# Optimization experiments

Measured on AMD Instinct MI355X. Metric: run time of the kernel, lower is better.

The kernel has to match this reference:

```python
import jax, jax.numpy as jnp
import numpy as np

EPS = 1e-5
KS = 3  # deformable kernel size
K2 = KS * KS


def conv2d(x, w, stride=1, padding=1):
    return jax.lax.conv_general_dilated(
        x, w, window_strides=(stride, stride),
        padding=[(padding, padding), (padding, padding)],
        dimension_numbers=("NCHW", "OIHW", "NCHW"))


def batchnorm(x, gamma, beta):
    # training-mode BN: batch statistics over (N, H, W)
    mean = jnp.mean(x, axis=(0, 2, 3), keepdims=True)
    var = jnp.var(x, axis=(0, 2, 3), keepdims=True)
    xhat = (x - mean) * jax.lax.rsqrt(var + EPS)
    return xhat * gamma[None, :, None, None] + beta[None, :, None, None]


def deform_conv(x, offsets, w, pad=1):
    # x: (B,C,H,W); offsets: (B,2*K2,H,W) -> first K2 channels = row (y)
    # offsets, next K2 = col (x) offsets; w: (O,C,KS,KS)
    B, C, H, W = x.shape
    xp = jnp.pad(x, ((0, 0), (0, 0), (pad, pad), (pad, pad)))
    Hp, Wp = H + 2 * pad, W + 2 * pad
    # base grid (center of each output pixel in padded coords)
    p0_y = jnp.arange(H, dtype=x.dtype) + pad            # (H,)
    p0_x = jnp.arange(W, dtype=x.dtype) + pad            # (W,)
    # kernel tap offsets in [-1, 0, 1]^2, row-major
    pn = jnp.stack(jnp.meshgrid(jnp.arange(KS) - pad, jnp.arange(KS) - pad,
                                indexing="ij"), axis=-1).reshape(K2, 2).astype(x.dtype)
    off = offsets.reshape(B, 2, K2, H, W)
    off_y = jnp.transpose(off[:, 0], (0, 2, 3, 1))       # (B,H,W,K2)
    off_x = jnp.transpose(off[:, 1], (0, 2, 3, 1))
    py = p0_y[None, :, None, None] + pn[:, 0][None, None, None, :] + off_y
    px = p0_x[None, None, :, None] + pn[:, 1][None, None, None, :] + off_x
    py = jnp.clip(py, 0.0, Hp - 1.0)
    px = jnp.clip(px, 0.0, Wp - 1.0)
    y0 = jnp.floor(py).astype(jnp.int32)
    x0 = jnp.floor(px).astype(jnp.int32)
    y1 = jnp.minimum(y0 + 1, Hp - 1)
    x1 = jnp.minimum(x0 + 1, Wp - 1)
    wy = (py - y0.astype(x.dtype))[:, None]              # (B,1,H,W,K2)
    wx = (px - x0.astype(x.dtype))[:, None]

    def gather(xb, yi, xi):                              # xb (C,Hp,Wp)
        return xb[:, yi, xi]                             # (C,H,W,K2)
    g = jax.vmap(gather)
    v00 = g(xp, y0, x0)
    v01 = g(xp, y0, x1)
    v10 = g(xp, y1, x0)
    v11 = g(xp, y1, x1)
    sampled = (v00 * (1 - wy) * (1 - wx) + v01 * (1 - wy) * wx +
               v10 * wy * (1 - wx) + v11 * wy * wx)      # (B,C,H,W,K2)
    return jnp.einsum("bchwk,ock->bohw", sampled, w.reshape(w.shape[0], C, K2))


def setup_inputs() -> dict:
    key = jax.random.key(0)
    ks = jax.random.split(key, 16)
    B, Cin, P, H, W = 64, 64, 64, 64, 64
    s = lambda k, shp, fan: jax.random.normal(k, shp, jnp.float32) * (fan ** -0.5)
    return {
        "x": jax.random.normal(ks[0], (B, Cin, H, W), jnp.float32),
        "conv1_w": s(ks[1], (P, Cin, 3, 3), Cin * 9),
        "bn1_g": jnp.ones((P,), jnp.float32), "bn1_b": jnp.zeros((P,), jnp.float32),
        "conv2_w": s(ks[2], (16, P, 1, 1), P),
        "bn2_g": jnp.ones((16,), jnp.float32), "bn2_b": jnp.zeros((16,), jnp.float32),
        "off_w": s(ks[3], (18, 16, 3, 3), 16 * 9) * 0.1,
        "off_b": jnp.zeros((18,), jnp.float32),
        "conv3_w": s(ks[4], (16, 16, 3, 3), 16 * 9),
        "bn3_g": jnp.ones((16,), jnp.float32), "bn3_b": jnp.zeros((16,), jnp.float32),
        "conv4_w": s(ks[5], (P, 16, 3, 3), 16 * 9),
        "bn4_g": jnp.ones((P,), jnp.float32), "bn4_b": jnp.zeros((P,), jnp.float32),
    }


def reference(x, conv1_w, bn1_g, bn1_b, conv2_w, bn2_g, bn2_b, off_w, off_b,
              conv3_w, bn3_g, bn3_b, conv4_w, bn4_g, bn4_b):
    out = jax.nn.relu(batchnorm(conv2d(x, conv1_w, 1, 1), bn1_g, bn1_b))
    out = jax.nn.relu(batchnorm(conv2d(out, conv2_w, 1, 0), bn2_g, bn2_b))
    offsets = conv2d(out, off_w, 1, 1) + off_b[None, :, None, None]
    out = jax.nn.relu(batchnorm(deform_conv(out, offsets, conv3_w), bn3_g, bn3_b))
    out = batchnorm(conv2d(out, conv4_w, 1, 1), bn4_g, bn4_b)
    out = out + x  # identity shortcut (stride=1, in_planes==planes)
    return jax.nn.relu(out)
```

## Files before the change

kernel.cpp:

```cpp
#include <hip/hip_runtime.h>

#define BN_N 262144.0f

typedef unsigned short u16;
typedef __attribute__((ext_vector_type(8))) short short8;
typedef __attribute__((ext_vector_type(4))) float floatx4;

#define RP1 4224
#define IS1 278784
#define RP2 1584
#define IS2 104544
#define H2P_TOTAL 6690816

static __device__ __forceinline__ u16 f2bf(float f) {
  union { float f; unsigned u; } v; v.f = f;
  unsigned u = v.u;
  return (u16)((u + 0x7FFFu + ((u >> 16) & 1u)) >> 16);
}
static __device__ __forceinline__ float bf2f(u16 h) {
  union { unsigned u; float f; } v; v.u = ((unsigned)h) << 16;
  return v.f;
}
static __device__ __forceinline__ void cp16(const u16* g, u16* l) {
  __builtin_amdgcn_global_load_lds((const __attribute__((address_space(1))) unsigned int*)g,
                                   (__attribute__((address_space(3))) unsigned int*)l, 16, 0, 0);
}

__global__ __launch_bounds__(256) void prep_w_k(const float* __restrict__ w1,
                                                u16* __restrict__ Bsw) {
  int d = blockIdx.x * 256 + threadIdx.x;
  int kin = d & 7, n = (d >> 3) & 63, kgrp = (d >> 9) & 3, kc = d >> 11;
  int k = kc * 32 + kgrp * 8 + kin;
  int tap = k >> 6, c = k & 63;
  Bsw[d] = f2bf(w1[n * 576 + c * 9 + tap]);
}

__global__ __launch_bounds__(256) void prep_w4_k(const float* __restrict__ w4,
                                                 u16* __restrict__ Bsw4) {
  int d = blockIdx.x * 256 + threadIdx.x;
  if (d >= 10240) return;
  int kin = d & 7, n = (d >> 3) & 63, lk = (d >> 9) & 3, kk = d >> 11;
  int tap = kk * 2 + (lk >> 1);
  int c = ((lk & 1) << 3) + kin;
  float v = (tap < 9) ? w4[n * 144 + c * 9 + tap] : 0.f;
  Bsw4[d] = f2bf(v);
}

__global__ __launch_bounds__(256) void prep_w3_k(const float* __restrict__ w3,
                                                 u16* __restrict__ Bsw3) {
  int d = blockIdx.x * 256 + threadIdx.x;
  if (d >= 2560) return;
  int kin = d & 7, n = (d >> 3) & 15, lk = (d >> 7) & 3, kk = d >> 9;
  int k = kk * 32 + lk * 8 + kin;
  int tap = k >> 4, c = k & 15;
  float v = (tap < 9) ? w3[n * 144 + c * 9 + tap] : 0.f;
  Bsw3[d] = f2bf(v);
}

__global__ __launch_bounds__(256) void prep_wo_k(const float* __restrict__ ow,
                                                 u16* __restrict__ BswO) {
  int d = blockIdx.x * 256 + threadIdx.x;
  if (d >= 5120) return;
  int kin = d & 7, n = (d >> 3) & 31, lk = (d >> 8) & 3, kk = d >> 10;
  int tap = kk * 2 + (lk >> 1);
  int c = ((lk & 1) << 3) + kin;
  float v = (tap < 9 && n < 18) ? ow[n * 144 + c * 9 + tap] : 0.f;
  BswO[d] = f2bf(v);
}

__global__ __launch_bounds__(256) void prep_x_k(const float* __restrict__ x,
                                                u16* __restrict__ xp) {
  int yp = blockIdx.x;
  int b = blockIdx.y;
  int tid = threadIdx.x;
  u16* rowbase = xp + (size_t)(b * 66 + yp) * RP1;
  if (yp == 0 || yp == 65) {
    for (int i = tid; i < RP1 / 4; i += 256)
      ((ushort4*)rowbase)[i] = make_ushort4(0, 0, 0, 0);
    return;
  }
  int y = yp - 1;
  __shared__ __align__(16) u16 s[64][72];
  for (int i = tid; i < 4096; i += 256) {
    int c = i >> 6, xx = i & 63;
    s[xx][c] = f2bf(x[((b * 64 + c) << 12) + (y << 6) + xx]);
  }
  if (tid < 128) {
    int c = tid & 63;
    int pxp = (tid >> 6) ? 65 : 0;
    rowbase[pxp * 64 + c] = 0;
  }
  __syncthreads();
  for (int j = tid; j < 512; j += 256) {
    int xx = j >> 3, chunk = j & 7;
    int pxp = xx + 1;
    int ph = chunk ^ (pxp & 7);
    *(short8*)(rowbase + pxp * 64 + ph * 8) = *(const short8*)(&s[xx][chunk * 8]);
  }
}

__global__ __launch_bounds__(256) void conv1_mfma(const u16* __restrict__ xp,
                                                  const u16* __restrict__ Bsw,
                                                  u16* __restrict__ h1,
                                                  float* __restrict__ sum1, float* __restrict__ sq1) {
  __shared__ __align__(16) u16 lA[25600];
  const int tid = threadIdx.x;
  const int w = tid >> 6, l = tid & 63;
  const int lm = l & 15, lk = l >> 4;
  const int b = blockIdx.x >> 4;
  const int y0 = (blockIdx.x & 15) << 2;
  const int y = y0 + w;
  const u16* src = xp + ((size_t)b * 66 + y0) * RP1;
  for (int seg = w; seg < 50; seg += 4)
    cp16(src + seg * 512 + l * 8, lA + seg * 512);
  __syncthreads();

  floatx4 acc[4][4];
#pragma unroll
  for (int mt = 0; mt < 4; ++mt)
#pragma unroll
    for (int nb = 0; nb < 4; ++nb)
      acc[mt][nb] = (floatx4){0.f, 0.f, 0.f, 0.f};

  short8 bC[4], bN[4];
#define BLOAD(KK, BV)                                                 \
  { const u16* bp_ = Bsw + ((((KK) * 4 + lk) * 64) + lm) * 8;         \
    BV[0] = *(const short8*)(bp_);                                    \
    BV[1] = *(const short8*)(bp_ + 128);                              \
    BV[2] = *(const short8*)(bp_ + 256);                              \
    BV[3] = *(const short8*)(bp_ + 384); }

  BLOAD(0, bC)
#pragma unroll
  for (int kk = 0; kk < 18; ++kk) {
    if (kk < 17) BLOAD(kk + 1, bN)
    const int tap = kk >> 1;
    const int dy = (tap < 3) ? 0 : ((tap < 6) ? 1 : 2);
    const int dx = tap - dy * 3;
    const int chunk = ((kk & 1) << 2) + lk;
    const int rowoff = (w + dy) * RP1;
    short8 aF[4];
#pragma unroll
    for (int mt = 0; mt < 4; ++mt) {
      int pxp = mt * 16 + lm + dx;
      int ph = chunk ^ (pxp & 7);
      aF[mt] = *(const short8*)(lA + rowoff + pxp * 64 + ph * 8);
    }
#pragma unroll
    for (int mt = 0; mt < 4; ++mt)
#pragma unroll
      for (int nb = 0; nb < 4; ++nb)
        acc[mt][nb] = __builtin_amdgcn_mfma_f32_16x16x32_bf16(aF[mt], bC[nb], acc[mt][nb], 0, 0, 0);
#pragma unroll
    for (int i = 0; i < 4; ++i) bC[i] = bN[i];
  }
#undef BLOAD

#pragma unroll
  for (int mt = 0; mt < 4; ++mt)
#pragma unroll
    for (int nb = 0; nb < 4; ++nb) {
      u16* dst = h1 + ((size_t)(b * 64 + nb * 16 + lm) << 12) + (y << 6) + mt * 16 + (lk << 2);
      floatx4 v = acc[mt][nb];
      *(ushort4*)dst = make_ushort4(f2bf(v.x), f2bf(v.y), f2bf(v.z), f2bf(v.w));
    }

  __syncthreads();
  float* LS = (float*)lA;
  float* LQ = LS + 256;
  float s[4], s2[4];
#pragma unroll
  for (int nb = 0; nb < 4; ++nb) {
    s[nb] = 0.f; s2[nb] = 0.f;
#pragma unroll
    for (int mt = 0; mt < 4; ++mt) {
      floatx4 a = acc[mt][nb];
      s[nb] += a.x + a.y + a.z + a.w;
      s2[nb] += a.x * a.x + a.y * a.y + a.z * a.z + a.w * a.w;
    }
    s[nb] += __shfl_xor(s[nb], 16, 64);  s[nb] += __shfl_xor(s[nb], 32, 64);
    s2[nb] += __shfl_xor(s2[nb], 16, 64); s2[nb] += __shfl_xor(s2[nb], 32, 64);
  }
  if (lk == 0) {
#pragma unroll
    for (int nb = 0; nb < 4; ++nb) { LS[w * 64 + nb * 16 + lm] = s[nb]; LQ[w * 64 + nb * 16 + lm] = s2[nb]; }
  }
  __syncthreads();
  if (tid < 64) atomicAdd(&sum1[tid], LS[tid] + LS[64 + tid] + LS[128 + tid] + LS[192 + tid]);
  else if (tid < 128) { int o = tid - 64; atomicAdd(&sq1[o], LQ[o] + LQ[64 + o] + LQ[128 + o] + LQ[192 + o]); }
}

__global__ __launch_bounds__(256) void conv2_k(const u16* __restrict__ h1,
                                               const float* __restrict__ w2,
                                               const float* __restrict__ sum1, const float* __restrict__ sq1,
                                               const float* __restrict__ g1, const float* __restrict__ b1,
                                               float* __restrict__ out,
                                               float* __restrict__ sum2, float* __restrict__ sq2) {
  __shared__ float s_wt[64 * 16];
  __shared__ float s_scale[64], s_shift[64];
  __shared__ float ls[4][16], lsq[4][16];
  int tid = threadIdx.x;
  for (int i = tid; i < 1024; i += 256) {
    int o = i >> 6, c = i & 63;
    s_wt[c * 16 + o] = w2[i];
  }
  if (tid < 64) {
    float m = sum1[tid] / BN_N;
    float var = sq1[tid] / BN_N - m * m;
    float sc = g1[tid] * rsqrtf(var + 1e-5f);
    s_scale[tid] = sc;
    s_shift[tid] = b1[tid] - m * sc;
  }
  __syncthreads();
  int p = blockIdx.x * 256 + tid;
  int b = p >> 12, r = p & 4095;
  const u16* src = h1 + ((size_t)b << 18) + r;
  float acc[16];
#pragma unroll
  for (int o = 0; o < 16; ++o) acc[o] = 0.f;
  for (int c = 0; c < 64; ++c) {
    float v = bf2f(src[c << 12]);
    v = fmaxf(v * s_scale[c] + s_shift[c], 0.f);
    const float* wp = &s_wt[c * 16];
    float4 w0 = *(const float4*)wp;
    float4 w1 = *(const float4*)(wp + 4);
    float4 w2v = *(const float4*)(wp + 8);
    float4 w3v = *(const float4*)(wp + 12);
    acc[0] += w0.x * v;  acc[1] += w0.y * v;  acc[2] += w0.z * v;  acc[3] += w0.w * v;
    acc[4] += w1.x * v;  acc[5] += w1.y * v;  acc[6] += w1.z * v;  acc[7] += w1.w * v;
    acc[8] += w2v.x * v; acc[9] += w2v.y * v; acc[10] += w2v.z * v; acc[11] += w2v.w * v;
    acc[12] += w3v.x * v; acc[13] += w3v.y * v; acc[14] += w3v.z * v; acc[15] += w3v.w * v;
  }
  float* dst = out + (size_t)p * 16;
#pragma unroll
  for (int c4 = 0; c4 < 4; ++c4)
    *(float4*)(dst + c4 * 4) = make_float4(acc[c4*4], acc[c4*4+1], acc[c4*4+2], acc[c4*4+3]);
  int lane = tid & 63, wv = tid >> 6;
#pragma unroll
  for (int o = 0; o < 16; ++o) {
    float s = acc[o], s2 = acc[o] * acc[o];
#pragma unroll
    for (int off = 32; off > 0; off >>= 1) {
      s += __shfl_down(s, off, 64);
      s2 += __shfl_down(s2, off, 64);
    }
    if (lane == 0) { ls[wv][o] = s; lsq[wv][o] = s2; }
  }
  __syncthreads();
  if (tid < 16) atomicAdd(&sum2[tid], ls[0][tid] + ls[1][tid] + ls[2][tid] + ls[3][tid]);
  else if (tid < 32) {
    int o = tid - 16;
    atomicAdd(&sq2[o], lsq[0][o] + lsq[1][o] + lsq[2][o] + lsq[3][o]);
  }
}

__global__ __launch_bounds__(256) void bnrelu2_k(const float* __restrict__ ws2,
                                                 const float* __restrict__ sum2, const float* __restrict__ sq2,
                                                 const float* __restrict__ g2, const float* __restrict__ b2,
                                                 u16* __restrict__ h2p) {
  __shared__ float s_scale[16], s_shift[16];
  int tid = threadIdx.x;
  if (tid < 16) {
    float m = sum2[tid] / BN_N;
    float var = sq2[tid] / BN_N - m * m;
    float sc = g2[tid] * rsqrtf(var + 1e-5f);
    s_scale[tid] = sc;
    s_shift[tid] = b2[tid] - m * sc;
  }
  __syncthreads();
  int p = blockIdx.x * 256 + tid;
  int b = p >> 12, r = p & 4095;
  int y = r >> 6, xx = r & 63;
  const float* src = ws2 + (size_t)p * 16;
  u16* dst = h2p + (size_t)(b * 66 + y + 1) * RP2 + (xx + 1) * 24;
#pragma unroll
  for (int c4 = 0; c4 < 4; ++c4) {
    float4 v = *(const float4*)(src + c4 * 4);
    u16 o0 = f2bf(fmaxf(v.x * s_scale[c4*4]   + s_shift[c4*4],   0.f));
    u16 o1 = f2bf(fmaxf(v.y * s_scale[c4*4+1] + s_shift[c4*4+1], 0.f));
    u16 o2 = f2bf(fmaxf(v.z * s_scale[c4*4+2] + s_shift[c4*4+2], 0.f));
    u16 o3 = f2bf(fmaxf(v.w * s_scale[c4*4+3] + s_shift[c4*4+3], 0.f));
    *(ushort4*)(dst + c4 * 4) = make_ushort4(o0, o1, o2, o3);
  }
}

__global__ __launch_bounds__(256) void offconv_mfma(const u16* __restrict__ h2p,
                                                    const u16* __restrict__ BswO,
                                                    const float* __restrict__ ob,
                                                    float* __restrict__ offs) {
  __shared__ __align__(16) u16 lA[9728];
  __shared__ __align__(16) u16 lB[5120];
  const int tid = threadIdx.x;
  const int w = tid >> 6, l = tid & 63;
  const int lm = l & 15, lk = l >> 4;
  const int b = blockIdx.x >> 4;
  const int y0 = (blockIdx.x & 15) << 2;
  const int y = y0 + w;
  const u16* src = h2p + ((size_t)b * 66 + y0) * RP2;
  for (int seg = w; seg < 19; seg += 4) cp16(src + seg * 512 + l * 8, lA + seg * 512);
  for (int seg = w; seg < 10; seg += 4) cp16(BswO + seg * 512 + l * 8, lB + seg * 512);
  __syncthreads();

  floatx4 acc[4][2];
#pragma unroll
  for (int mt = 0; mt < 4; ++mt)
#pragma unroll
    for (int nb = 0; nb < 2; ++nb)
      acc[mt][nb] = (floatx4){0.f, 0.f, 0.f, 0.f};

#pragma unroll
  for (int kk = 0; kk < 5; ++kk) {
    int tap = kk * 2 + (lk >> 1);
    if (tap > 8) tap = 8;
    const int dy = tap / 3, dx = tap - dy * 3;
    const int c0 = (lk & 1) << 3;
    const int rowoff = (w + dy) * RP2;
    short8 aF[4], bF[2];
#pragma unroll
    for (int mt = 0; mt < 4; ++mt)
      aF[mt] = *(const short8*)(lA + rowoff + (mt * 16 + lm + dx) * 24 + c0);
    const u16* bp = lB + (((kk * 4 + lk) * 32) + lm) * 8;
    bF[0] = *(const short8*)(bp);
    bF[1] = *(const short8*)(bp + 128);
#pragma unroll
    for (int mt = 0; mt < 4; ++mt)
#pragma unroll
      for (int nb = 0; nb < 2; ++nb)
        acc[mt][nb] = __builtin_amdgcn_mfma_f32_16x16x32_bf16(aF[mt], bF[nb], acc[mt][nb], 0, 0, 0);
  }

#pragma unroll
  for (int mt = 0; mt < 4; ++mt)
#pragma unroll
    for (int nb = 0; nb < 2; ++nb) {
      int oc = nb * 16 + lm;
      if (oc < 18) {
        float bias = ob[oc];
        floatx4 v = acc[mt][nb];
        v.x += bias; v.y += bias; v.z += bias; v.w += bias;
        float* dst = offs + (size_t)b * 73728 + (oc << 12) + (y << 6) + mt * 16 + (lk << 2);
        *(floatx4*)dst = v;
      }
    }
}

__global__ __launch_bounds__(256) void deform_mfma(const u16* __restrict__ h2p,
                                                   const float* __restrict__ offs,
                                                   const u16* __restrict__ Bsw3,
                                                   float* __restrict__ out,
                                                   float* __restrict__ sum3, float* __restrict__ sq3) {
  const int tid = threadIdx.x;
  const int w = tid >> 6, l = tid & 63;
  const int lm = l & 15, lk = l >> 4;
  const int pbase = blockIdx.x * 256 + w * 64;
  const int b = pbase >> 12;
  const u16* img = h2p + (size_t)b * IS2;
  const float* offp = offs + (size_t)b * 73728;

  short8 bf[5];
#pragma unroll
  for (int kk = 0; kk < 5; ++kk)
    bf[kk] = *(const short8*)(Bsw3 + (((kk * 4 + lk) * 16) + lm) * 8);

  floatx4 acc[4];
#pragma unroll
  for (int mt = 0; mt < 4; ++mt) acc[mt] = (floatx4){0.f, 0.f, 0.f, 0.f};

#pragma unroll
  for (int mt = 0; mt < 4; ++mt) {
    const int p = pbase + mt * 16 + lm;
    const int r = p & 4095;
    const int y = r >> 6, x = r & 63;
#pragma unroll
    for (int kk = 0; kk < 5; ++kk) {
      const int k0 = kk * 32 + lk * 8;
      int tap = k0 >> 4;
      const int c0 = k0 & 15;
      if (tap > 8) tap = 8;
      const int dy = tap / 3, dx = tap - dy * 3;
      float offy = offp[(tap << 12) + r];
      float offx = offp[((tap + 9) << 12) + r];
      float py = (float)(y + dy) + offy;
      float px = (float)(x + dx) + offx;
      py = fminf(fmaxf(py, 0.f), 65.f);
      px = fminf(fmaxf(px, 0.f), 65.f);
      float y0f = floorf(py), x0f = floorf(px);
      int y0 = (int)y0f, x0 = (int)x0f;
      int y1 = min(y0 + 1, 65), x1 = min(x0 + 1, 65);
      float wy = py - y0f, wx = px - x0f;
      float w00 = (1.f - wy) * (1.f - wx), w01 = (1.f - wy) * wx;
      float w10 = wy * (1.f - wx),         w11 = wy * wx;
      short8 v00 = *(const short8*)(img + (y0 * 66 + x0) * 24 + c0);
      short8 v01 = *(const short8*)(img + (y0 * 66 + x1) * 24 + c0);
      short8 v10 = *(const short8*)(img + (y1 * 66 + x0) * 24 + c0);
      short8 v11 = *(const short8*)(img + (y1 * 66 + x1) * 24 + c0);
      short8 a;
#pragma unroll
      for (int j = 0; j < 8; ++j) {
        float s = bf2f((u16)v00[j]) * w00 + bf2f((u16)v01[j]) * w01
                + bf2f((u16)v10[j]) * w10 + bf2f((u16)v11[j]) * w11;
        a[j] = (short)f2bf(s);
      }
      acc[mt] = __builtin_amdgcn_mfma_f32_16x16x32_bf16(a, bf[kk], acc[mt], 0, 0, 0);
    }
  }

  float s = 0.f, s2 = 0.f;
#pragma unroll
  for (int mt = 0; mt < 4; ++mt) {
    floatx4 a = acc[mt];
    s += a.x + a.y + a.z + a.w;
    s2 += a.x * a.x + a.y * a.y + a.z * a.z + a.w * a.w;
#pragma unroll
    for (int reg = 0; reg < 4; ++reg) {
      int pp = pbase + mt * 16 + lk * 4 + reg;
      out[(size_t)pp * 16 + lm] = acc[mt][reg];
    }
  }
  __shared__ float ls[4][16], lsq[4][16];
  s += __shfl_xor(s, 16, 64);  s += __shfl_xor(s, 32, 64);
  s2 += __shfl_xor(s2, 16, 64); s2 += __shfl_xor(s2, 32, 64);
  if (lk == 0) { ls[w][lm] = s; lsq[w][lm] = s2; }
  __syncthreads();
  if (tid < 16) atomicAdd(&sum3[tid], ls[0][tid] + ls[1][tid] + ls[2][tid] + ls[3][tid]);
  else if (tid < 32) {
    int o = tid - 16;
    atomicAdd(&sq3[o], lsq[0][o] + lsq[1][o] + lsq[2][o] + lsq[3][o]);
  }
}

__global__ __launch_bounds__(256) void bnrelu3_k(const float* __restrict__ wsd,
                                                 const float* __restrict__ sum3, const float* __restrict__ sq3,
                                                 const float* __restrict__ g3, const float* __restrict__ b3,
                                                 u16* __restrict__ h3p) {
  __shared__ float s_scale[16], s_shift[16];
  int tid = threadIdx.x;
  if (tid < 16) {
    float m = sum3[tid] / BN_N;
    float var = sq3[tid] / BN_N - m * m;
    float sc = g3[tid] * rsqrtf(var + 1e-5f);
    s_scale[tid] = sc;
    s_shift[tid] = b3[tid] - m * sc;
  }
  __syncthreads();
  int p = blockIdx.x * 256 + tid;
  int b = p >> 12, r = p & 4095;
  int y = r >> 6, xx = r & 63;
  const float* src = wsd + (size_t)p * 16;
  u16* dst = h3p + (size_t)(b * 66 + y + 1) * RP2 + (xx + 1) * 24;
#pragma unroll
  for (int c4 = 0; c4 < 4; ++c4) {
    float4 v = *(const float4*)(src + c4 * 4);
    u16 o0 = f2bf(fmaxf(v.x * s_scale[c4*4]   + s_shift[c4*4],   0.f));
    u16 o1 = f2bf(fmaxf(v.y * s_scale[c4*4+1] + s_shift[c4*4+1], 0.f));
    u16 o2 = f2bf(fmaxf(v.z * s_scale[c4*4+2] + s_shift[c4*4+2], 0.f));
    u16 o3 = f2bf(fmaxf(v.w * s_scale[c4*4+3] + s_shift[c4*4+3], 0.f));
    *(ushort4*)(dst + c4 * 4) = make_ushort4(o0, o1, o2, o3);
  }
}

__global__ __launch_bounds__(256) void conv4_mfma(const u16* __restrict__ h3p,
                                                  const u16* __restrict__ Bsw4,
                                                  u16* __restrict__ h4,
                                                  float* __restrict__ sum4, float* __restrict__ sq4) {
  __shared__ __align__(16) u16 lA[9728];
  __shared__ __align__(16) u16 lB[10240];
  const int tid = threadIdx.x;
  const int w = tid >> 6, l = tid & 63;
  const int lm = l & 15, lk = l >> 4;
  const int b = blockIdx.x >> 4;
  const int y0 = (blockIdx.x & 15) << 2;
  const int y = y0 + w;
  const u16* src = h3p + ((size_t)b * 66 + y0) * RP2;
  for (int seg = w; seg < 19; seg += 4) cp16(src + seg * 512 + l * 8, lA + seg * 512);
  for (int seg = w; seg < 20; seg += 4) cp16(Bsw4 + seg * 512 + l * 8, lB + seg * 512);
  __syncthreads();

  floatx4 acc[4][4];
#pragma unroll
  for (int mt = 0; mt < 4; ++mt)
#pragma unroll
    for (int nb = 0; nb < 4; ++nb)
      acc[mt][nb] = (floatx4){0.f, 0.f, 0.f, 0.f};

#pragma unroll
  for (int kk = 0; kk < 5; ++kk) {
    int tap = kk * 2 + (lk >> 1);
    if (tap > 8) tap = 8;
    const int dy = tap / 3, dx = tap - dy * 3;
    const int c0 = (lk & 1) << 3;
    const int rowoff = (w + dy) * RP2;
    short8 aF[4], bF[4];
#pragma unroll
    for (int mt = 0; mt < 4; ++mt)
      aF[mt] = *(const short8*)(lA + rowoff + (mt * 16 + lm + dx) * 24 + c0);
    const u16* bp = lB + (((kk * 4 + lk) * 64) + lm) * 8;
    bF[0] = *(const short8*)(bp);
    bF[1] = *(const short8*)(bp + 128);
    bF[2] = *(const short8*)(bp + 256);
    bF[3] = *(const short8*)(bp + 384);
#pragma unroll
    for (int mt = 0; mt < 4; ++mt)
#pragma unroll
      for (int nb = 0; nb < 4; ++nb)
        acc[mt][nb] = __builtin_amdgcn_mfma_f32_16x16x32_bf16(aF[mt], bF[nb], acc[mt][nb], 0, 0, 0);
  }

#pragma unroll
  for (int mt = 0; mt < 4; ++mt)
#pragma unroll
    for (int nb = 0; nb < 4; ++nb) {
      u16* dst = h4 + ((size_t)(b * 64 + nb * 16 + lm) << 12) + (y << 6) + mt * 16 + (lk << 2);
      floatx4 v = acc[mt][nb];
      *(ushort4*)dst = make_ushort4(f2bf(v.x), f2bf(v.y), f2bf(v.z), f2bf(v.w));
    }

  __syncthreads();
  float* LS = (float*)lA;
  float* LQ = LS + 256;
  float s[4], s2[4];
#pragma unroll
  for (int nb = 0; nb < 4; ++nb) {
    s[nb] = 0.f; s2[nb] = 0.f;
#pragma unroll
    for (int mt = 0; mt < 4; ++mt) {
      floatx4 a = acc[mt][nb];
      s[nb] += a.x + a.y + a.z + a.w;
      s2[nb] += a.x * a.x + a.y * a.y + a.z * a.z + a.w * a.w;
    }
    s[nb] += __shfl_xor(s[nb], 16, 64);  s[nb] += __shfl_xor(s[nb], 32, 64);
    s2[nb] += __shfl_xor(s2[nb], 16, 64); s2[nb] += __shfl_xor(s2[nb], 32, 64);
  }
  if (lk == 0) {
#pragma unroll
    for (int nb = 0; nb < 4; ++nb) { LS[w * 64 + nb * 16 + lm] = s[nb]; LQ[w * 64 + nb * 16 + lm] = s2[nb]; }
  }
  __syncthreads();
  if (tid < 64) atomicAdd(&sum4[tid], LS[tid] + LS[64 + tid] + LS[128 + tid] + LS[192 + tid]);
  else if (tid < 128) { int o = tid - 64; atomicAdd(&sq4[o], LQ[o] + LQ[64 + o] + LQ[128 + o] + LQ[192 + o]); }
}

__global__ __launch_bounds__(256) void final_k(const u16* __restrict__ h4,
                                               float* __restrict__ out,
                                               const float* __restrict__ x,
                                               const float* __restrict__ sum4, const float* __restrict__ sq4,
                                               const float* __restrict__ g4, const float* __restrict__ b4) {
  __shared__ float s_scale[64], s_shift[64];
  int tid = threadIdx.x;
  if (tid < 64) {
    float m = sum4[tid] / BN_N;
    float var = sq4[tid] / BN_N - m * m;
    float sc = g4[tid] * rsqrtf(var + 1e-5f);
    s_scale[tid] = sc;
    s_shift[tid] = b4[tid] - m * sc;
  }
  __syncthreads();
  int i = (blockIdx.x * 256 + tid) * 4;
  int c = (i >> 12) & 63;
  ushort4 q = *(const ushort4*)(h4 + i);
  float4 xv = *(const float4*)(x + i);
  float sc = s_scale[c], sh = s_shift[c];
  float4 v;
  v.x = fmaxf(bf2f(q.x) * sc + sh + xv.x, 0.f);
  v.y = fmaxf(bf2f(q.y) * sc + sh + xv.y, 0.f);
  v.z = fmaxf(bf2f(q.z) * sc + sh + xv.z, 0.f);
  v.w = fmaxf(bf2f(q.w) * sc + sh + xv.w, 0.f);
  *(float4*)(out + i) = v;
}

extern "C" void kernel_launch(void* const* d_in, const int* in_sizes, int n_in,
                              void* d_out, int out_size, void* d_ws, size_t ws_size,
                              hipStream_t stream) {
  const float* x  = (const float*)d_in[0];
  const float* w1 = (const float*)d_in[1];
  const float* g1 = (const float*)d_in[2];
  const float* b1 = (const float*)d_in[3];
  const float* w2 = (const float*)d_in[4];
  const float* g2 = (const float*)d_in[5];
  const float* b2 = (const float*)d_in[6];
  const float* ow = (const float*)d_in[7];
  const float* ob = (const float*)d_in[8];
  const float* w3 = (const float*)d_in[9];
  const float* g3 = (const float*)d_in[10];
  const float* b3 = (const float*)d_in[11];
  const float* w4 = (const float*)d_in[12];
  const float* g4 = (const float*)d_in[13];
  const float* b4 = (const float*)d_in[14];
  float* out = (float*)d_out;
  float* ws = (float*)d_ws;

  float* offs = ws;
  float* wsd  = offs + 4718592;
  float* ws2  = wsd + 4194304;
  float* h2pf = ws2 + 4194304;
  float* stats = h2pf + 4460544;
  float* sum1 = stats, *sq1 = stats + 64;
  float* sum2 = stats + 128, *sq2 = stats + 144;
  float* sum3 = stats + 160, *sq3 = stats + 176;
  float* sum4 = stats + 192, *sq4 = stats + 256;
  u16* xp   = (u16*)ws;
  u16* Bsw  = (u16*)(stats + 320);
  u16* Bsw4 = Bsw + 36864;
  u16* Bsw3 = Bsw4 + 10240;
  u16* BswO = Bsw3 + 2560;
  u16* h2p  = (u16*)h2pf;
  u16* h4   = (u16*)offs;
  u16* h1   = (u16*)out;

  hipMemsetAsync(stats, 0, 320 * sizeof(float), stream);
  hipMemsetAsync(h2p, 0, (size_t)H2P_TOTAL * sizeof(u16), stream);

  prep_w_k<<<144, 256, 0, stream>>>(w1, Bsw);
  prep_w4_k<<<40, 256, 0, stream>>>(w4, Bsw4);
  prep_w3_k<<<10, 256, 0, stream>>>(w3, Bsw3);
  prep_wo_k<<<20, 256, 0, stream>>>(ow, BswO);
  prep_x_k<<<dim3(66, 64), 256, 0, stream>>>(x, xp);
  conv1_mfma<<<1024, 256, 0, stream>>>(xp, Bsw, h1, sum1, sq1);
  conv2_k<<<1024, 256, 0, stream>>>(h1, w2, sum1, sq1, g1, b1, ws2, sum2, sq2);
  bnrelu2_k<<<1024, 256, 0, stream>>>(ws2, sum2, sq2, g2, b2, h2p);
  offconv_mfma<<<1024, 256, 0, stream>>>(h2p, BswO, ob, offs);
  deform_mfma<<<1024, 256, 0, stream>>>(h2p, offs, Bsw3, wsd, sum3, sq3);
  bnrelu3_k<<<1024, 256, 0, stream>>>(wsd, sum3, sq3, g3, b3, h2p );
  conv4_mfma<<<1024, 256, 0, stream>>>(h2p, Bsw4, h4, sum4, sq4);
  final_k<<<16384, 256, 0, stream>>>(h4, out, x, sum4, sq4, g4, b4);
}
```

Before: 338.4 us.

## Read conv1 A operands straight from global memory instead of staging in LDS

The conv1 MFMA kernel no longer copies the padded input rows into a 50 KB LDS tile; each wave loads its A fragments directly from global memory, relying on cache for the reuse across the three row taps. The B weight double-buffering is replaced by plain per-iteration loads, and launch bounds request 4 blocks per SM now that LDS use is small. This removes the LDS fill and its barrier and lets more blocks run at once, at the cost of repeated global/L2 traffic and exposed load latency inside the MFMA loop.

Result: slower. 358.8 us (+6.0%).

```diff
diff --git a/kernel.cpp b/kernel.cpp
--- a/kernel.cpp
+++ b/kernel.cpp
@@ -99,21 +99,17 @@
   }
 }
 
-__global__ __launch_bounds__(256) void conv1_mfma(const u16* __restrict__ xp,
-                                                  const u16* __restrict__ Bsw,
-                                                  u16* __restrict__ h1,
-                                                  float* __restrict__ sum1, float* __restrict__ sq1) {
-  __shared__ __align__(16) u16 lA[25600];
+__global__ __launch_bounds__(256, 4) void conv1_mfma(const u16* __restrict__ xp,
+                                                     const u16* __restrict__ Bsw,
+                                                     u16* __restrict__ h1,
+                                                     float* __restrict__ sum1, float* __restrict__ sq1) {
   const int tid = threadIdx.x;
   const int w = tid >> 6, l = tid & 63;
   const int lm = l & 15, lk = l >> 4;
   const int b = blockIdx.x >> 4;
   const int y0 = (blockIdx.x & 15) << 2;
   const int y = y0 + w;
-  const u16* src = xp + ((size_t)b * 66 + y0) * RP1;
-  for (int seg = w; seg < 50; seg += 4)
-    cp16(src + seg * 512 + l * 8, lA + seg * 512);
-  __syncthreads();
+  const u16* base = xp + ((size_t)b * 66 + y) * RP1;
 
   floatx4 acc[4][4];
 #pragma unroll
@@ -122,39 +118,31 @@
     for (int nb = 0; nb < 4; ++nb)
       acc[mt][nb] = (floatx4){0.f, 0.f, 0.f, 0.f};
 
-  short8 bC[4], bN[4];
-#define BLOAD(KK, BV)                                                 \
-  { const u16* bp_ = Bsw + ((((KK) * 4 + lk) * 64) + lm) * 8;         \
-    BV[0] = *(const short8*)(bp_);                                    \
-    BV[1] = *(const short8*)(bp_ + 128);                              \
-    BV[2] = *(const short8*)(bp_ + 256);                              \
-    BV[3] = *(const short8*)(bp_ + 384); }
-
-  BLOAD(0, bC)
 #pragma unroll
   for (int kk = 0; kk < 18; ++kk) {
-    if (kk < 17) BLOAD(kk + 1, bN)
     const int tap = kk >> 1;
     const int dy = (tap < 3) ? 0 : ((tap < 6) ? 1 : 2);
     const int dx = tap - dy * 3;
     const int chunk = ((kk & 1) << 2) + lk;
-    const int rowoff = (w + dy) * RP1;
-    short8 aF[4];
+    const u16* rp = base + dy * RP1;
+    short8 aF[4], bF[4];
+    const u16* bp_ = Bsw + ((((kk) * 4 + lk) * 64) + lm) * 8;
+    bF[0] = *(const short8*)(bp_);
+    bF[1] = *(const short8*)(bp_ + 128);
+    bF[2] = *(const short8*)(bp_ + 256);
+    bF[3] = *(const short8*)(bp_ + 384);
 #pragma unroll
     for (int mt = 0; mt < 4; ++mt) {
       int pxp = mt * 16 + lm + dx;
       int ph = chunk ^ (pxp & 7);
-      aF[mt] = *(const short8*)(lA + rowoff + pxp * 64 + ph * 8);
+      aF[mt] = *(const short8*)(rp + pxp * 64 + ph * 8);
     }
 #pragma unroll
     for (int mt = 0; mt < 4; ++mt)
 #pragma unroll
       for (int nb = 0; nb < 4; ++nb)
-        acc[mt][nb] = __builtin_amdgcn_mfma_f32_16x16x32_bf16(aF[mt], bC[nb], acc[mt][nb], 0, 0, 0);
-#pragma unroll
-    for (int i = 0; i < 4; ++i) bC[i] = bN[i];
-  }
-#undef BLOAD
+        acc[mt][nb] = __builtin_amdgcn_mfma_f32_16x16x32_bf16(aF[mt], bF[nb], acc[mt][nb], 0, 0, 0);
+  }
 
 #pragma unroll
   for (int mt = 0; mt < 4; ++mt)
@@ -165,9 +153,7 @@
       *(ushort4*)dst = make_ushort4(f2bf(v.x), f2bf(v.y), f2bf(v.z), f2bf(v.w));
     }
 
-  __syncthreads();
-  float* LS = (float*)lA;
-  float* LQ = LS + 256;
+  __shared__ float LS[256], LQ[256];
   float s[4], s2[4];
 #pragma unroll
   for (int nb = 0; nb < 4; ++nb) {
```
